# Kernel optimization log

Hardware: AMD Instinct MI355X
Metric: run time of the kernel (lower is better)

## Reference

```python
import jax, jax.numpy as jnp
import numpy as np

B = 256   # batch size
NX = 256  # spatial grid points
T = 100   # time steps in u
TEMP = 1.0
LAM = 0.9  # lambda_1


def _advection(u, dt, dx, coeff):
    d = (jnp.roll(u, 1, axis=1) - jnp.roll(u, -1, axis=1)) * u
    return coeff[:, None, None] * dt[:, None, None] * d / (2.0 * dx[:, None, None])


def _diffusion(u, dt, dx, coeff):
    d = jnp.roll(u, 1, axis=1) + jnp.roll(u, -1, axis=1) - 2.0 * u
    return -(coeff[:, None, None] * dt[:, None, None] * d / dx[:, None, None] ** 2)


def _linear_advection(u, dt, dx, coeff):
    num = u - jnp.roll(u, -1, axis=1)
    return -coeff[:, None, None] * dt[:, None, None] * num / dx[:, None, None]


def _anchored_l2(xi, xj, ui, uj, dt, dx, coeff):
    # us[i, j, :] = ui[j, :, -1] - uj[i, :, -2]  -> [2B, 2B, NX]
    us = ui[..., -1][None, :, :] - uj[..., -2][:, None, :]
    adv = _advection(xi, dt, dx, coeff[:, 0])
    diff = _diffusion(xi, dt, dx, coeff[:, 1])
    dis = _linear_advection(xi, dt, dx, coeff[:, 2])
    updates = (adv + diff + dis)[..., 0]  # [2B, NX]
    pd = (xi[..., 0] + updates)[:, None, :] - xj[..., 0][None, :, :]  # [2B, 2B, NX]
    d = us - pd
    return jnp.sum(d * d, axis=-1)  # norm(dim=-1)**2


def reference(x1, x2, u, dt, dx, vs):
    bs = x1.shape[0]
    # _pde_similarity(vs): pairwise sqrt(sum|vi*vj|) / max(||vi||, ||vj||)
    prod = jnp.sqrt(jnp.sum(jnp.abs(vs[None, :, :] * vs[:, None, :]), axis=-1))
    nv = jnp.linalg.norm(vs, axis=-1)
    sim = prod / jnp.maximum(nv[:, None], nv[None, :])
    ss = jnp.nan_to_num(1.0 - LAM * sim, nan=0.0)
    # drop diagonal (row-major, static indices), then tile to [2B, 2(B-1)]
    ri, ci = np.nonzero(~np.eye(bs, dtype=bool))
    ss = ss[ri, ci].reshape(bs, bs - 1)
    ss = jnp.tile(ss, (2, 2))
    reps = jnp.concatenate([x2, x1], axis=0)           # [2B, NX, 1, 1]
    reps = reps.reshape(2 * bs, -1, reps.shape[-1])    # flatten(1,2) -> [2B, NX, 1]
    u2 = jnp.concatenate([u, u], axis=0)
    dt2 = jnp.concatenate([dt, dt], axis=0)
    vs2 = jnp.concatenate([vs, vs], axis=0)
    simmat = _anchored_l2(reps, reps, u2, u2, dt2, dx, vs2)  # [2B, 2B]
    l_pos = jnp.diagonal(simmat, offset=bs)
    r_pos = jnp.diagonal(simmat, offset=-bs)
    pos = jnp.concatenate([l_pos, r_pos]).reshape(2 * bs, 1)
    m = np.eye(2 * bs) + np.eye(2 * bs, k=-bs) + np.eye(2 * bs, k=bs)
    nri, nci = np.nonzero((1 - m).astype(bool))
    neg = simmat[nri, nci].reshape(2 * bs, 2 * bs - 2) * ss
    logits = jnp.concatenate([pos, neg], axis=1) / TEMP
    lp = jax.nn.log_softmax(logits, axis=-1)
    # CrossEntropyLoss(reduction='sum') with all labels == 0
    return -jnp.sum(lp[:, 0]) / (2 * bs)


def setup_inputs():
    key = jax.random.key(0)
    k1, k2, k3, k4, k5 = jax.random.split(key, 5)
    return {
        'x1': jax.random.normal(k1, (B, NX, 1, 1), dtype=jnp.float32),
        'x2': jax.random.normal(k2, (B, NX, 1, 1), dtype=jnp.float32),
        'u': jax.random.normal(k3, (B, NX, T), dtype=jnp.float32),
        'dt': jax.random.uniform(k4, (B,), dtype=jnp.float32),
        'dx': jnp.ones((1,), dtype=jnp.float32),
        'vs': jax.random.normal(k5, (B, 3), dtype=jnp.float32),
    }
```

## Files before the change

kernel.cpp:

```cpp
#include <hip/hip_runtime.h>
#include <math.h>

#define BQ 256
#define NXQ 256
#define TQ 100
#define N2 512
#define TILE 32
#define PITCH 257

__global__ __launch_bounds__(256) void prep_kernel(
    const float* __restrict__ x1, const float* __restrict__ x2,
    const float* __restrict__ u, const float* __restrict__ dt,
    const float* __restrict__ dx, const float* __restrict__ vs,
    float* __restrict__ A, float* __restrict__ C, float* __restrict__ SS) {
  int blk = blockIdx.x;
  int t = threadIdx.x;
  if (blk < N2) {
    int r = blk;
    int b = r & (BQ - 1);
    const float* xr = (r < BQ ? x2 : x1);
    __shared__ float ws[NXQ];
    ws[t] = xr[b * NXQ + t];
    __syncthreads();
    float w0 = ws[t];
    float wm = ws[(t + NXQ - 1) & (NXQ - 1)];
    float wp = ws[(t + 1) & (NXQ - 1)];
    float dtv = dt[b];
    float dxv = dx[0];
    float c0 = vs[b * 3 + 0], c1 = vs[b * 3 + 1], c2 = vs[b * 3 + 2];
    float adv = c0 * dtv * (wm - wp) * w0 / (2.0f * dxv);
    float dif = -(c1 * dtv * (wm + wp - 2.0f * w0) / (dxv * dxv));
    float dis = -c2 * dtv * (w0 - wp) / dxv;
    float upd = adv + dif + dis;
    const float* urow = u + (size_t)(b * NXQ + t) * TQ;
    A[r * NXQ + t] = urow[TQ - 1] + w0;
    C[r * NXQ + t] = urow[TQ - 2] + w0 + upd;
  } else {
    int i = blk - N2;
    int j = t;
    float vi0 = vs[i * 3], vi1 = vs[i * 3 + 1], vi2 = vs[i * 3 + 2];
    float vj0 = vs[j * 3], vj1 = vs[j * 3 + 1], vj2 = vs[j * 3 + 2];
    float nvi = sqrtf(vi0 * vi0 + vi1 * vi1 + vi2 * vi2);
    float nvj = sqrtf(vj0 * vj0 + vj1 * vj1 + vj2 * vj2);
    float prod = sqrtf(fabsf(vi0 * vj0) + fabsf(vi1 * vj1) + fabsf(vi2 * vj2));
    float sim = prod / fmaxf(nvi, nvj);
    float ssv = 1.0f - 0.9f * sim;
    if (isnan(ssv)) ssv = 0.0f;
    SS[i * BQ + j] = ssv;
  }
}

__global__ __launch_bounds__(256) void dist_kernel(const float* __restrict__ A,
                                                   const float* __restrict__ C,
                                                   float* __restrict__ SIM) {
  __shared__ float At[TILE * PITCH];
  __shared__ float Ct[TILE * PITCH];
  int t = threadIdx.x;
  int i0 = blockIdx.y * TILE;
  int j0 = blockIdx.x * TILE;
  for (int k = 0; k < TILE * NXQ / 256; k++) {
    int idx = k * 256 + t;
    int row = idx >> 8;
    int col = idx & (NXQ - 1);
    At[row * PITCH + col] = A[(j0 + row) * NXQ + col];
    Ct[row * PITCH + col] = C[(i0 + row) * NXQ + col];
  }
  __syncthreads();
  int ii = t >> 3;
  int jj = (t & 7) << 2;
  float acc0 = 0.f, acc1 = 0.f, acc2 = 0.f, acc3 = 0.f;
  for (int x = 0; x < NXQ; x++) {
    float cv = Ct[ii * PITCH + x];
    float d0 = At[(jj + 0) * PITCH + x] - cv;
    float d1 = At[(jj + 1) * PITCH + x] - cv;
    float d2 = At[(jj + 2) * PITCH + x] - cv;
    float d3 = At[(jj + 3) * PITCH + x] - cv;
    acc0 = fmaf(d0, d0, acc0);
    acc1 = fmaf(d1, d1, acc1);
    acc2 = fmaf(d2, d2, acc2);
    acc3 = fmaf(d3, d3, acc3);
  }
  float4 v = make_float4(acc0, acc1, acc2, acc3);
  *(float4*)&SIM[(i0 + ii) * N2 + j0 + jj] = v;
}

__global__ __launch_bounds__(256) void row_kernel(const float* __restrict__ SIM,
                                                  const float* __restrict__ SS,
                                                  double* __restrict__ ROW) {
  int r = blockIdx.x;
  int t = threadIdx.x;
  int rb = r & (BQ - 1);
  int jstar = (r + BQ) & (N2 - 1);
  float posval = SIM[r * N2 + jstar];
  float ssv = SS[rb * BQ + t];
  float v0, v1;
  {
    int j = t;
    if (j == jstar)                  v0 = posval;
    else if ((j & (BQ - 1)) == rb)   v0 = -INFINITY;
    else                             v0 = SIM[r * N2 + j] * ssv;
  }
  {
    int j = t + BQ;
    if (j == jstar)                  v1 = posval;
    else if ((j & (BQ - 1)) == rb)   v1 = -INFINITY;
    else                             v1 = SIM[r * N2 + j] * ssv;
  }
  float m = fmaxf(v0, v1);
  for (int off = 32; off > 0; off >>= 1) m = fmaxf(m, __shfl_down(m, off, 64));
  __shared__ float wmax[4];
  __shared__ double wsum[4];
  int wave = t >> 6, lane = t & 63;
  if (lane == 0) wmax[wave] = m;
  __syncthreads();
  float M = fmaxf(fmaxf(wmax[0], wmax[1]), fmaxf(wmax[2], wmax[3]));
  double s = 0.0;
  if (v0 != -INFINITY) s += exp((double)(v0 - M));
  if (v1 != -INFINITY) s += exp((double)(v1 - M));
  for (int off = 32; off > 0; off >>= 1) s += __shfl_down(s, off, 64);
  if (lane == 0) wsum[wave] = s;
  __syncthreads();
  if (t == 0) {
    double S = wsum[0] + wsum[1] + wsum[2] + wsum[3];
    ROW[r] = (double)M + log(S) - (double)posval;
  }
}

__global__ __launch_bounds__(256) void final_kernel(const double* __restrict__ ROW,
                                                    float* __restrict__ out) {
  int t = threadIdx.x;
  double s = ROW[t] + ROW[t + 256];
  for (int off = 32; off > 0; off >>= 1) s += __shfl_down(s, off, 64);
  __shared__ double wsum[4];
  int wave = t >> 6, lane = t & 63;
  if (lane == 0) wsum[wave] = s;
  __syncthreads();
  if (t == 0) {
    double S = wsum[0] + wsum[1] + wsum[2] + wsum[3];
    out[0] = (float)(S / (double)N2);
  }
}

extern "C" void kernel_launch(void* const* d_in, const int* in_sizes, int n_in,
                              void* d_out, int out_size, void* d_ws, size_t ws_size,
                              hipStream_t stream) {
  const float* x1 = (const float*)d_in[0];
  const float* x2 = (const float*)d_in[1];
  const float* u  = (const float*)d_in[2];
  const float* dt = (const float*)d_in[3];
  const float* dx = (const float*)d_in[4];
  const float* vs = (const float*)d_in[5];
  char* ws = (char*)d_ws;
  float*  SIM = (float*)(ws + 0);
  float*  A   = (float*)(ws + 1048576);
  float*  C   = (float*)(ws + 1572864);
  float*  SS  = (float*)(ws + 2097152);
  double* ROW = (double*)(ws + 2359296);
  float* out = (float*)d_out;

  prep_kernel<<<N2 + BQ, 256, 0, stream>>>(x1, x2, u, dt, dx, vs, A, C, SS);
  dim3 g2(N2 / TILE, N2 / TILE);
  dist_kernel<<<g2, 256, 0, stream>>>(A, C, SIM);
  row_kernel<<<N2, 256, 0, stream>>>(SIM, SS, ROW);
  final_kernel<<<1, 256, 0, stream>>>(ROW, out);
}
```

Baseline: 94.63 us.

## Merge row-softmax and final reduction via atomics, retile distance kernel

The prep kernel now handles both x1 and x2 rows per block and reads the two needed u values with one float2 load. It also zeroes the output. The distance kernel uses 2x2 register tiles over two 128-wide shared-memory chunks with float2 loads. The row kernel assigns one wave per row, computes log-sum-exp in float instead of double, and accumulates the loss with an atomicAdd, which removes the final kernel launch. The trade-offs are lower numerical precision and a float atomic accumulation order that is not deterministic.

Result: slower. 98.38 us (+4.0%).

```diff
diff --git a/kernel.cpp b/kernel.cpp
--- a/kernel.cpp
+++ b/kernel.cpp
@@ -5,38 +5,47 @@
 #define NXQ 256
 #define TQ 100
 #define N2 512
-#define TILE 32
-#define PITCH 257
+#define DP 130
 
 __global__ __launch_bounds__(256) void prep_kernel(
     const float* __restrict__ x1, const float* __restrict__ x2,
     const float* __restrict__ u, const float* __restrict__ dt,
     const float* __restrict__ dx, const float* __restrict__ vs,
-    float* __restrict__ A, float* __restrict__ C, float* __restrict__ SS) {
+    float* __restrict__ A, float* __restrict__ C, float* __restrict__ SS,
+    float* __restrict__ out) {
   int blk = blockIdx.x;
   int t = threadIdx.x;
-  if (blk < N2) {
-    int r = blk;
-    int b = r & (BQ - 1);
-    const float* xr = (r < BQ ? x2 : x1);
-    __shared__ float ws[NXQ];
-    ws[t] = xr[b * NXQ + t];
+  if (blk == 0 && t == 0) out[0] = 0.0f;
+  if (blk < BQ) {
+    int b = blk;
+    __shared__ float w1[NXQ], w2[NXQ];
+    w2[t] = x2[b * NXQ + t];
+    w1[t] = x1[b * NXQ + t];
     __syncthreads();
-    float w0 = ws[t];
-    float wm = ws[(t + NXQ - 1) & (NXQ - 1)];
-    float wp = ws[(t + 1) & (NXQ - 1)];
+    int tm = (t + NXQ - 1) & (NXQ - 1);
+    int tp = (t + 1) & (NXQ - 1);
     float dtv = dt[b];
     float dxv = dx[0];
     float c0 = vs[b * 3 + 0], c1 = vs[b * 3 + 1], c2 = vs[b * 3 + 2];
-    float adv = c0 * dtv * (wm - wp) * w0 / (2.0f * dxv);
-    float dif = -(c1 * dtv * (wm + wp - 2.0f * w0) / (dxv * dxv));
-    float dis = -c2 * dtv * (w0 - wp) / dxv;
-    float upd = adv + dif + dis;
-    const float* urow = u + (size_t)(b * NXQ + t) * TQ;
-    A[r * NXQ + t] = urow[TQ - 1] + w0;
-    C[r * NXQ + t] = urow[TQ - 2] + w0 + upd;
+    float2 uu = *(const float2*)&u[(size_t)(b * NXQ + t) * TQ + (TQ - 2)];
+    {
+      float w0 = w2[t], wm = w2[tm], wp = w2[tp];
+      float upd = c0 * dtv * (wm - wp) * w0 / (2.0f * dxv)
+                - c1 * dtv * (wm + wp - 2.0f * w0) / (dxv * dxv)
+                - c2 * dtv * (w0 - wp) / dxv;
+      A[b * NXQ + t] = uu.y + w0;
+      C[b * NXQ + t] = uu.x + w0 + upd;
+    }
+    {
+      float w0 = w1[t], wm = w1[tm], wp = w1[tp];
+      float upd = c0 * dtv * (wm - wp) * w0 / (2.0f * dxv)
+                - c1 * dtv * (wm + wp - 2.0f * w0) / (dxv * dxv)
+                - c2 * dtv * (w0 - wp) / dxv;
+      A[(b + BQ) * NXQ + t] = uu.y + w0;
+      C[(b + BQ) * NXQ + t] = uu.x + w0 + upd;
+    }
   } else {
-    int i = blk - N2;
+    int i = blk - BQ;
     int j = t;
     float vi0 = vs[i * 3], vi1 = vs[i * 3 + 1], vi2 = vs[i * 3 + 2];
     float vj0 = vs[j * 3], vj1 = vs[j * 3 + 1], vj2 = vs[j * 3 + 2];
@@ -53,91 +62,82 @@
 __global__ __launch_bounds__(256) void dist_kernel(const float* __restrict__ A,
                                                    const float* __restrict__ C,
                                                    float* __restrict__ SIM) {
-  __shared__ float At[TILE * PITCH];
-  __shared__ float Ct[TILE * PITCH];
+  __shared__ float At[32 * DP];
+  __shared__ float Ct[32 * DP];
   int t = threadIdx.x;
-  int i0 = blockIdx.y * TILE;
-  int j0 = blockIdx.x * TILE;
-  for (int k = 0; k < TILE * NXQ / 256; k++) {
-    int idx = k * 256 + t;
-    int row = idx >> 8;
-    int col = idx & (NXQ - 1);
-    At[row * PITCH + col] = A[(j0 + row) * NXQ + col];
-    Ct[row * PITCH + col] = C[(i0 + row) * NXQ + col];
+  int i0 = blockIdx.y * 32;
+  int j0 = blockIdx.x * 32;
+  int ci = (t >> 4) * 2;
+  int aj = (t & 15) * 2;
+  float acc00 = 0.f, acc01 = 0.f, acc10 = 0.f, acc11 = 0.f;
+  for (int ch = 0; ch < 2; ++ch) {
+    #pragma unroll
+    for (int k = 0; k < 8; ++k) {
+      int fidx = k * 256 + t;
+      int row = fidx >> 6;
+      int xi = (fidx & 63) * 2;
+      float2 av = *(const float2*)&A[(j0 + row) * NXQ + ch * 128 + xi];
+      float2 cv = *(const float2*)&C[(i0 + row) * NXQ + ch * 128 + xi];
+      *(float2*)&At[row * DP + xi] = av;
+      *(float2*)&Ct[row * DP + xi] = cv;
+    }
+    __syncthreads();
+    #pragma unroll 4
+    for (int x = 0; x < 128; x += 2) {
+      float2 a0 = *(float2*)&At[aj * DP + x];
+      float2 a1 = *(float2*)&At[(aj + 1) * DP + x];
+      float2 c0 = *(float2*)&Ct[ci * DP + x];
+      float2 c1 = *(float2*)&Ct[(ci + 1) * DP + x];
+      float d;
+      d = a0.x - c0.x; acc00 = fmaf(d, d, acc00);
+      d = a0.y - c0.y; acc00 = fmaf(d, d, acc00);
+      d = a1.x - c0.x; acc01 = fmaf(d, d, acc01);
+      d = a1.y - c0.y; acc01 = fmaf(d, d, acc01);
+      d = a0.x - c1.x; acc10 = fmaf(d, d, acc10);
+      d = a0.y - c1.y; acc10 = fmaf(d, d, acc10);
+      d = a1.x - c1.x; acc11 = fmaf(d, d, acc11);
+      d = a1.y - c1.y; acc11 = fmaf(d, d, acc11);
+    }
+    __syncthreads();
   }
-  __syncthreads();
-  int ii = t >> 3;
-  int jj = (t & 7) << 2;
-  float acc0 = 0.f, acc1 = 0.f, acc2 = 0.f, acc3 = 0.f;
-  for (int x = 0; x < NXQ; x++) {
-    float cv = Ct[ii * PITCH + x];
-    float d0 = At[(jj + 0) * PITCH + x] - cv;
-    float d1 = At[(jj + 1) * PITCH + x] - cv;
-    float d2 = At[(jj + 2) * PITCH + x] - cv;
-    float d3 = At[(jj + 3) * PITCH + x] - cv;
-    acc0 = fmaf(d0, d0, acc0);
-    acc1 = fmaf(d1, d1, acc1);
-    acc2 = fmaf(d2, d2, acc2);
-    acc3 = fmaf(d3, d3, acc3);
-  }
-  float4 v = make_float4(acc0, acc1, acc2, acc3);
-  *(float4*)&SIM[(i0 + ii) * N2 + j0 + jj] = v;
+  *(float2*)&SIM[(i0 + ci) * N2 + j0 + aj]     = make_float2(acc00, acc01);
+  *(float2*)&SIM[(i0 + ci + 1) * N2 + j0 + aj] = make_float2(acc10, acc11);
 }
 
 __global__ __launch_bounds__(256) void row_kernel(const float* __restrict__ SIM,
                                                   const float* __restrict__ SS,
-                                                  double* __restrict__ ROW) {
-  int r = blockIdx.x;
+                                                  float* __restrict__ out) {
   int t = threadIdx.x;
+  int wave = t >> 6, lane = t & 63;
+  int r = blockIdx.x * 4 + wave;
   int rb = r & (BQ - 1);
   int jstar = (r + BQ) & (N2 - 1);
-  float posval = SIM[r * N2 + jstar];
-  float ssv = SS[rb * BQ + t];
-  float v0, v1;
-  {
-    int j = t;
-    if (j == jstar)                  v0 = posval;
-    else if ((j & (BQ - 1)) == rb)   v0 = -INFINITY;
-    else                             v0 = SIM[r * N2 + j] * ssv;
+  const float* srow = SIM + r * N2;
+  float pos = srow[jstar];
+  float v[8];
+  #pragma unroll
+  for (int k = 0; k < 8; ++k) {
+    int j = lane + k * 64;
+    float s = srow[j];
+    float w = SS[rb * BQ + (j & (BQ - 1))];
+    float val = s * w;
+    if (j == jstar) val = pos;
+    else if ((j & (BQ - 1)) == rb) val = -INFINITY;
+    v[k] = val;
   }
-  {
-    int j = t + BQ;
-    if (j == jstar)                  v1 = posval;
-    else if ((j & (BQ - 1)) == rb)   v1 = -INFINITY;
-    else                             v1 = SIM[r * N2 + j] * ssv;
-  }
-  float m = fmaxf(v0, v1);
-  for (int off = 32; off > 0; off >>= 1) m = fmaxf(m, __shfl_down(m, off, 64));
-  __shared__ float wmax[4];
-  __shared__ double wsum[4];
-  int wave = t >> 6, lane = t & 63;
-  if (lane == 0) wmax[wave] = m;
-  __syncthreads();
-  float M = fmaxf(fmaxf(wmax[0], wmax[1]), fmaxf(wmax[2], wmax[3]));
-  double s = 0.0;
-  if (v0 != -INFINITY) s += exp((double)(v0 - M));
-  if (v1 != -INFINITY) s += exp((double)(v1 - M));
-  for (int off = 32; off > 0; off >>= 1) s += __shfl_down(s, off, 64);
-  if (lane == 0) wsum[wave] = s;
-  __syncthreads();
-  if (t == 0) {
-    double S = wsum[0] + wsum[1] + wsum[2] + wsum[3];
-    ROW[r] = (double)M + log(S) - (double)posval;
-  }
-}
-
-__global__ __launch_bounds__(256) void final_kernel(const double* __restrict__ ROW,
-                                                    float* __restrict__ out) {
-  int t = threadIdx.x;
-  double s = ROW[t] + ROW[t + 256];
-  for (int off = 32; off > 0; off >>= 1) s += __shfl_down(s, off, 64);
-  __shared__ double wsum[4];
-  int wave = t >> 6, lane = t & 63;
-  if (lane == 0) wsum[wave] = s;
-  __syncthreads();
-  if (t == 0) {
-    double S = wsum[0] + wsum[1] + wsum[2] + wsum[3];
-    out[0] = (float)(S / (double)N2);
+  float m = v[0];
+  #pragma unroll
+  for (int k = 1; k < 8; ++k) m = fmaxf(m, v[k]);
+  #pragma unroll
+  for (int off = 32; off > 0; off >>= 1) m = fmaxf(m, __shfl_xor(m, off, 64));
+  float S = 0.f;
+  #pragma unroll
+  for (int k = 0; k < 8; ++k) S += expf(v[k] - m);
+  #pragma unroll
+  for (int off = 32; off > 0; off >>= 1) S += __shfl_xor(S, off, 64);
+  if (lane == 0) {
+    double lse = (double)m + log((double)S);
+    atomicAdd(out, (float)((lse - (double)pos) * (1.0 / (double)N2)));
   }
 }
 
@@ -151,16 +151,14 @@
   const float* dx = (const float*)d_in[4];
   const float* vs = (const float*)d_in[5];
   char* ws = (char*)d_ws;
-  float*  SIM = (float*)(ws + 0);
-  float*  A   = (float*)(ws + 1048576);
-  float*  C   = (float*)(ws + 1572864);
-  float*  SS  = (float*)(ws + 2097152);
-  double* ROW = (double*)(ws + 2359296);
+  float* SIM = (float*)(ws + 0);
+  float* A   = (float*)(ws + 1048576);
+  float* C   = (float*)(ws + 1572864);
+  float* SS  = (float*)(ws + 2097152);
   float* out = (float*)d_out;
 
-  prep_kernel<<<N2 + BQ, 256, 0, stream>>>(x1, x2, u, dt, dx, vs, A, C, SS);
-  dim3 g2(N2 / TILE, N2 / TILE);
+  prep_kernel<<<N2, 256, 0, stream>>>(x1, x2, u, dt, dx, vs, A, C, SS, out);
+  dim3 g2(N2 / 32, N2 / 32);
   dist_kernel<<<g2, 256, 0, stream>>>(A, C, SIM);
-  row_kernel<<<N2, 256, 0, stream>>>(SIM, SS, ROW);
-  final_kernel<<<1, 256, 0, stream>>>(ROW, out);
+  row_kernel<<<N2 / 4, 256, 0, stream>>>(SIM, SS, out);
 }
```
